# Kernel tuning notes

Measured on AMD Instinct MI355X. Metric: run time of the kernel, lower is better.

## Reference

```python
import jax, jax.numpy as jnp
import numpy as np

B, S, D = 16, 1024, 1024      # batch, seq_len (== max_ctx_k), input_dim (== embed_dim)
H = 1                          # num_heads (module's v-reshape requires 1)
E = 1024                       # embed_dim
TEMP = 1.0
EPS = 1e-12


def setup_inputs() -> dict:
    key = jax.random.key(0)
    ks = jax.random.split(key, 10)
    x = jax.random.normal(ks[0], (B, S, D), dtype=jnp.float32)
    mask = jax.random.randint(ks[1], (B, S, S), 0, 2, dtype=jnp.int32)
    # parameters (xavier-ish scales)
    Wqkv = jax.random.normal(ks[2], (2 * E, D), dtype=jnp.float32) * (1.0 / np.sqrt(D))
    bqkv = jax.random.normal(ks[3], (2 * E,), dtype=jnp.float32) * 0.02
    Wctx = jax.random.normal(ks[4], (2 * S, S), dtype=jnp.float32) * (1.0 / np.sqrt(S))
    bctx = jax.random.normal(ks[5], (2 * S,), dtype=jnp.float32) * 0.02
    Wf = jax.random.normal(ks[6], (1, 2), dtype=jnp.float32)
    bf = jax.random.normal(ks[7], (1,), dtype=jnp.float32) * 0.02
    Wo = jax.random.normal(ks[8], (D, 2 * D), dtype=jnp.float32) * (1.0 / np.sqrt(2 * D))
    bo = jax.random.normal(ks[9], (D,), dtype=jnp.float32) * 0.02
    return {"x": x, "mask": mask, "Wqkv": Wqkv, "bqkv": bqkv, "Wctx": Wctx,
            "bctx": bctx, "Wf": Wf, "bf": bf, "Wo": Wo, "bo": bo}


def reference(x, mask, Wqkv, bqkv, Wctx, bctx, Wf, bf, Wo, bo):
    head_dim = E // H
    # qkv projection -> (B, H, S, 2*head_dim)
    qkv = (jnp.einsum('bsd,ed->bse', x, Wqkv) + bqkv)
    qkv = qkv.reshape(B, S, H, 2 * head_dim).transpose(0, 2, 1, 3)
    q, k = jnp.split(qkv, 2, axis=-1)
    # v is just x per head (num_heads == 1)
    v = x.reshape(B, S, H, D).transpose(0, 2, 1, 3)          # (B, H, S, D)
    # self-attention scores (NOT scaled by sqrt(d_k), faithful to source)
    self_attn = jnp.einsum('bhqd,bhkd->bhqk', q, k)           # (B, H, S, S)
    # adjacency-derived context scores
    adj = jnp.einsum('bqd,bkd->bqk', x, x)[:, None]           # (B, 1, S, S)
    ctx_qk = jnp.einsum('bhqs,ts->bhqt', adj, Wctx) + bctx    # (B, 1, S, 2S)
    ctx_q, ctx_k = jnp.split(ctx_qk, 2, axis=-1)
    ctx_q = ctx_q / jnp.maximum(jnp.linalg.norm(ctx_q, axis=-1, keepdims=True), EPS)
    ctx_k = ctx_k / jnp.maximum(jnp.linalg.norm(ctx_k, axis=-1, keepdims=True), EPS)
    ctx_attn = jnp.einsum('bhqs,bhks->bhqk', ctx_q, ctx_k)    # (B, 1, S, S)
    # learned fuse of the two score maps: Linear(2 -> 1)
    attn = self_attn * Wf[0, 0] + ctx_attn * Wf[0, 1] + bf[0]
    attn = jax.nn.softmax(attn / TEMP, axis=-1)
    # post-softmax masking + L1 renorm
    m = (mask[:, None] != 0)                                  # (B, 1, S, S)
    attn = jnp.where(m, attn, 0.0)
    attn = attn / jnp.maximum(jnp.sum(jnp.abs(attn), axis=-1, keepdims=True), EPS)
    # value matmul and output projection
    values = jnp.einsum('bhqk,bhkd->bhqd', attn, v)           # (B, H, S, D)
    values = values.transpose(0, 2, 1, 3).reshape(B, S, D)
    o = jnp.einsum('bse,de->bsd', jnp.concatenate([x, values], axis=-1), Wo) + bo
    return o
```

## Files before the change

### kernel.cpp

```cpp
#include <hip/hip_runtime.h>
#include <hip/hip_bf16.h>

#define BB 16
#define SS 1024
#define DD 1024

typedef __hip_bfloat16 bf;
using s8v   = __attribute__((ext_vector_type(8))) short;
using f32x4 = __attribute__((ext_vector_type(4))) float;
using u16x4 = __attribute__((ext_vector_type(4))) unsigned short;

__device__ __forceinline__ void gload16(const bf* g, unsigned short* l)
{
    __builtin_amdgcn_global_load_lds(
        (const __attribute__((address_space(1))) void*)g,
        (__attribute__((address_space(3))) void*)l,
        16, 0, 0);
}

template <int EP>
__global__ __launch_bounds__(512, 2) void gemm256(
    const bf* __restrict__ A, long sA, int lda, int segA,
    const bf* __restrict__ B, long sB, int ldb, int segB,
    float* __restrict__ C, bf* __restrict__ Cb,
    bf* __restrict__ qp, bf* __restrict__ kp,
    long sC, int ldc, int K,
    const float* __restrict__ bias,
    const float* __restrict__ alpha_ptr, int alpha_idx,
    const float* __restrict__ addc_ptr,
    int accumulate)
{
    __shared__ __align__(16) unsigned short lds[65536];
    unsigned short* Asm = lds;
    unsigned short* Bsm = lds + 32768;

    const int gx = gridDim.x, gy = gridDim.y;
    const int nwg = gx * gy * (int)gridDim.z;
    int lid = blockIdx.x + gx * (blockIdx.y + gy * blockIdx.z);
    lid = (lid & 7) * (nwg >> 3) + (lid >> 3);
    const int bx = lid % gx;
    const int rem = lid / gx;
    const int by = rem % gy;
    const int bz = rem / gy;

    const int tid = threadIdx.x;
    const int w = tid >> 6, l = tid & 63;
    const int wm = w >> 2, wn = w & 3;
    const int lm = l & 15, quad = l >> 4;
    const int bh = wn >> 1;
    const int bl0 = (wn & 1) * 64;

    const int m0 = by * 256, n0 = bx * 256;
    const bf* Ab = A + (long)bz * sA;
    const bf* Bb = B + (long)bz * sB;

    const int srow = w * 16 + (l >> 3);
    const int scol = ((l & 7) ^ (l >> 3)) << 3;
    const long aoff0 = (long)srow * lda + scol;
    const long aoff1 = (long)(srow + 8) * lda + scol;
    const long boff0 = (long)srow * ldb + scol;
    const long boff1 = (long)(srow + 8) * ldb + scol;
    const int ldst = w * 1024;

    auto stageA = [&](int tt, int h) {
        const int kk = ((tt & 15) << 6) +
                       ((((unsigned)segA >> ((tt >> 4) << 3)) & 0xffu) << 10);
        const bf* g = Ab + (long)(m0 + h * 128) * lda + kk;
        unsigned short* d = Asm + (((tt & 1) << 1) + h) * 8192 + ldst;
        gload16(g + aoff0, d);
        gload16(g + aoff1, d + 512);
    };
    auto stageB = [&](int tt, int h) {
        const int kk = ((tt & 15) << 6) +
                       ((((unsigned)segB >> ((tt >> 4) << 3)) & 0xffu) << 10);
        const bf* g = Bb + (long)(n0 + h * 128) * ldb + kk;
        unsigned short* d = Bsm + (((tt & 1) << 1) + h) * 8192 + ldst;
        gload16(g + boff0, d);
        gload16(g + boff1, d + 512);
    };
    auto rdA = [&](int d, int rl, int ks) -> s8v {
        const int off = rl * 64 + (((ks << 5) + (quad << 3)) ^ ((rl & 7) << 3));
        return *(const s8v*)(Asm + ((d << 1) + wm) * 8192 + off);
    };
    auto rdB = [&](int d, int bl, int ks) -> s8v {
        const int off = bl * 64 + (((ks << 5) + (quad << 3)) ^ ((bl & 7) << 3));
        return *(const s8v*)(Bsm + ((d << 1) + bh) * 8192 + off);
    };

    f32x4 acc[8][4];
#pragma unroll
    for (int i = 0; i < 8; ++i)
#pragma unroll
        for (int j = 0; j < 4; ++j)
            acc[i][j] = (f32x4){0.f, 0.f, 0.f, 0.f};

    const int NT = K >> 6;

    stageA(0, 0); stageA(0, 1); stageB(0, 0); stageB(0, 1);
    asm volatile("s_waitcnt vmcnt(4)" ::: "memory");
    stageA(1, 0); stageA(1, 1); stageB(1, 0);
    asm volatile("s_waitcnt vmcnt(6)" ::: "memory");
    __builtin_amdgcn_s_barrier();

    s8v a[8], b[4];
    for (int t = 0; t < NT; ++t) {
        const int d = t & 1;
#pragma unroll
        for (int mf = 0; mf < 4; ++mf) {
            a[mf * 2]     = rdA(d, mf * 16 + lm, 0);
            a[mf * 2 + 1] = rdA(d, mf * 16 + lm, 1);
        }
#pragma unroll
        for (int nf = 0; nf < 2; ++nf) {
            b[nf * 2]     = rdB(d, bl0 + nf * 16 + lm, 0);
            b[nf * 2 + 1] = rdB(d, bl0 + nf * 16 + lm, 1);
        }
        if (t + 1 < NT) stageB(t + 1, 1);
        __builtin_amdgcn_s_barrier();
        __builtin_amdgcn_s_setprio(1);
#pragma unroll
        for (int mf = 0; mf < 4; ++mf)
#pragma unroll
            for (int nf = 0; nf < 2; ++nf) {
                acc[mf][nf] = __builtin_amdgcn_mfma_f32_16x16x32_bf16(a[mf*2],   b[nf*2],   acc[mf][nf], 0, 0, 0);
                acc[mf][nf] = __builtin_amdgcn_mfma_f32_16x16x32_bf16(a[mf*2+1], b[nf*2+1], acc[mf][nf], 0, 0, 0);
            }
        __builtin_amdgcn_s_setprio(0);
        __builtin_amdgcn_s_barrier();
#pragma unroll
        for (int nf = 0; nf < 2; ++nf) {
            b[nf * 2]     = rdB(d, bl0 + (nf + 2) * 16 + lm, 0);
            b[nf * 2 + 1] = rdB(d, bl0 + (nf + 2) * 16 + lm, 1);
        }
        __builtin_amdgcn_s_barrier();
        __builtin_amdgcn_s_setprio(1);
#pragma unroll
        for (int mf = 0; mf < 4; ++mf)
#pragma unroll
            for (int nf = 0; nf < 2; ++nf) {
                acc[mf][nf+2] = __builtin_amdgcn_mfma_f32_16x16x32_bf16(a[mf*2],   b[nf*2],   acc[mf][nf+2], 0, 0, 0);
                acc[mf][nf+2] = __builtin_amdgcn_mfma_f32_16x16x32_bf16(a[mf*2+1], b[nf*2+1], acc[mf][nf+2], 0, 0, 0);
            }
        __builtin_amdgcn_s_setprio(0);
        __builtin_amdgcn_s_barrier();
#pragma unroll
        for (int mf = 0; mf < 4; ++mf) {
            a[mf * 2]     = rdA(d, 64 + mf * 16 + lm, 0);
            a[mf * 2 + 1] = rdA(d, 64 + mf * 16 + lm, 1);
        }
        if (t + 2 < NT) { stageA(t + 2, 0); stageA(t + 2, 1); }
        __builtin_amdgcn_s_barrier();
        __builtin_amdgcn_s_setprio(1);
#pragma unroll
        for (int mf = 0; mf < 4; ++mf)
#pragma unroll
            for (int nf = 0; nf < 2; ++nf) {
                acc[mf+4][nf+2] = __builtin_amdgcn_mfma_f32_16x16x32_bf16(a[mf*2],   b[nf*2],   acc[mf+4][nf+2], 0, 0, 0);
                acc[mf+4][nf+2] = __builtin_amdgcn_mfma_f32_16x16x32_bf16(a[mf*2+1], b[nf*2+1], acc[mf+4][nf+2], 0, 0, 0);
            }
        __builtin_amdgcn_s_setprio(0);
        __builtin_amdgcn_s_barrier();
#pragma unroll
        for (int nf = 0; nf < 2; ++nf) {
            b[nf * 2]     = rdB(d, bl0 + nf * 16 + lm, 0);
            b[nf * 2 + 1] = rdB(d, bl0 + nf * 16 + lm, 1);
        }
        if (t + 2 < NT) {
            stageB(t + 2, 0);
            asm volatile("s_waitcnt vmcnt(6)" ::: "memory");
        } else {
            asm volatile("s_waitcnt vmcnt(0)" ::: "memory");
        }
        __builtin_amdgcn_s_barrier();
        __builtin_amdgcn_s_setprio(1);
#pragma unroll
        for (int mf = 0; mf < 4; ++mf)
#pragma unroll
            for (int nf = 0; nf < 2; ++nf) {
                acc[mf+4][nf] = __builtin_amdgcn_mfma_f32_16x16x32_bf16(a[mf*2],   b[nf*2],   acc[mf+4][nf], 0, 0, 0);
                acc[mf+4][nf] = __builtin_amdgcn_mfma_f32_16x16x32_bf16(a[mf*2+1], b[nf*2+1], acc[mf+4][nf], 0, 0, 0);
            }
        __builtin_amdgcn_s_setprio(0);
        __builtin_amdgcn_s_barrier();
    }

    const float alpha = alpha_ptr ? alpha_ptr[alpha_idx] : 1.0f;
    const float addc  = addc_ptr ? addc_ptr[0] : 0.0f;
    float* Cp = C ? C + (long)bz * sC : nullptr;
    bf* Cbp = (EP == 1) ? Cb + (long)bz * sC : nullptr;
    bf* qpz = (EP == 2 || EP == 3) ? qp + (long)bz * sC : nullptr;
    bf* kpz = (EP == 2 || EP == 3) ? kp + (long)bz * sC : nullptr;

#pragma unroll
    for (int mf = 0; mf < 8; ++mf) {
#pragma unroll
        for (int nf = 0; nf < 4; ++nf) {
            const int cidx = n0 + wn * 64 + nf * 16 + lm;
            const float bv = bias ? bias[cidx] : 0.0f;
            const long rbase = m0 + wm * 128 + mf * 16 + quad * 4;
#pragma unroll
            for (int r = 0; r < 4; ++r) {
                const long row = rbase + r;
                if (EP == 2) {
                    float v = acc[mf][nf][r] + bv;
                    if (cidx < 1024) {
                        v *= alpha;
                        bf hi = __float2bfloat16(v);
                        bf lo = __float2bfloat16(v - __bfloat162float(hi));
                        qpz[row * 3072 + cidx] = hi;
                        qpz[row * 3072 + 1024 + cidx] = lo;
                    } else {
                        const int c = cidx - 1024;
                        bf hi = __float2bfloat16(v);
                        bf lo = __float2bfloat16(v - __bfloat162float(hi));
                        kpz[row * 3072 + c] = hi;
                        kpz[row * 3072 + 1024 + c] = lo;
                    }
                } else if (EP == 3) {
                    const float v = acc[mf][nf][r] + bv;
                    const bf h = __float2bfloat16(v);
                    if (cidx < 1024) qpz[row * 3072 + 2048 + cidx] = h;
                    else             kpz[row * 3072 + 2048 + (cidx - 1024)] = h;
                } else {
                    float v = alpha * acc[mf][nf][r] + addc + bv;
                    const long off = row * (long)ldc + cidx;
                    if (EP == 1) {
                        Cbp[off] = __float2bfloat16(v);
                    } else {
                        if (accumulate) v += Cp[off];
                        Cp[off] = v;
                    }
                }
            }
        }
    }
}

__device__ inline float blockReduceSum(float v, float* red)
{
#pragma unroll
    for (int off = 32; off > 0; off >>= 1) v += __shfl_xor(v, off, 64);
    __syncthreads();
    if ((threadIdx.x & 63) == 0) red[threadIdx.x >> 6] = v;
    __syncthreads();
    return red[0] + red[1] + red[2] + red[3];
}

__device__ inline float blockReduceMax(float v, float* red)
{
#pragma unroll
    for (int off = 32; off > 0; off >>= 1) v = fmaxf(v, __shfl_xor(v, off, 64));
    __syncthreads();
    if ((threadIdx.x & 63) == 0) red[threadIdx.x >> 6] = v;
    __syncthreads();
    return fmaxf(fmaxf(red[0], red[1]), fmaxf(red[2], red[3]));
}

__device__ inline void split_bf16(float v, bf& hi, bf& lo)
{
    hi = __float2bfloat16(v);
    lo = __float2bfloat16(v - __bfloat162float(hi));
}

__global__ __launch_bounds__(256) void prep_wqkv_kernel(
    const float* __restrict__ W, bf* __restrict__ wq2)
{
    long i = (long)blockIdx.x * 256 + threadIdx.x;
    long r = i >> 10; int c = (int)(i & 1023);
    bf hi, lo; split_bf16(W[i], hi, lo);
    wq2[r * 2048 + c] = hi;
    wq2[r * 2048 + 1024 + c] = lo;
}

__global__ __launch_bounds__(256) void conv_kernel(
    const float* __restrict__ src, bf* __restrict__ dst, int cols, int src_ld, long n)
{
    long i = (long)blockIdx.x * 256 + threadIdx.x;
    if (i >= n) return;
    long r = i / cols; int c = (int)(i % cols);
    dst[i] = __float2bfloat16(src[r * src_ld + c]);
}

__global__ __launch_bounds__(256) void conv_x_kernel(
    const float* __restrict__ x, bf* __restrict__ xhl, bf* __restrict__ xT1)
{
    __shared__ float t[32][33];
    const int b = blockIdx.z;
    const int c0 = blockIdx.x * 32, r0 = blockIdx.y * 32;
    const int tx = threadIdx.x & 31, ty = threadIdx.x >> 5;
    const float* xb = x + (long)b * SS * DD;
    bf* xhlb = xhl + (long)b * SS * 2048;
#pragma unroll
    for (int p = 0; p < 4; ++p) {
        const int r = ty + 8 * p;
        const float v = xb[(long)(r0 + r) * DD + c0 + tx];
        t[r][tx] = v;
        bf hi, lo; split_bf16(v, hi, lo);
        xhlb[(long)(r0 + r) * 2048 + c0 + tx] = hi;
        xhlb[(long)(r0 + r) * 2048 + 1024 + c0 + tx] = lo;
    }
    __syncthreads();
#pragma unroll
    for (int p = 0; p < 4; ++p) {
        const int rr = ty + 8 * p;
        xT1[(long)b * DD * SS + (long)(c0 + rr) * SS + r0 + tx] =
            __float2bfloat16(t[tx][rr]);
    }
}

__global__ __launch_bounds__(256) void l2norm_fuse_kernel(
    bf* __restrict__ q3, bf* __restrict__ k3, const float* __restrict__ Wf)
{
    __shared__ float red[4];
    const long row = blockIdx.x >> 1;
    const int half = blockIdx.x & 1;
    bf* p = (half ? k3 : q3) + row * 3072 + 2048;
    const int t = threadIdx.x;

    const u16x4 u = *reinterpret_cast<const u16x4*>(p + 4 * t);
    float v[4];
    float ss = 0.0f;
#pragma unroll
    for (int i = 0; i < 4; ++i) {
        unsigned short us = u[i];
        v[i] = __bfloat162float(*reinterpret_cast<const bf*>(&us));
        ss = fmaf(v[i], v[i], ss);
    }
    ss = blockReduceSum(ss, red);
    const float inv = 1.0f / fmaxf(sqrtf(ss), 1e-12f);
    const float scale = half ? inv : inv * Wf[1];
    u16x4 o;
#pragma unroll
    for (int i = 0; i < 4; ++i) {
        bf h = __float2bfloat16(v[i] * scale);
        o[i] = *reinterpret_cast<unsigned short*>(&h);
    }
    *reinterpret_cast<u16x4*>(p + 4 * t) = o;
}

__global__ __launch_bounds__(256) void softmax_mask_kernel(
    const float* __restrict__ attn, const int* __restrict__ mask, bf* __restrict__ attn_bf)
{
    __shared__ float red[4];
    const long row = blockIdx.x;
    const float* p = attn + row * SS;
    const int* mrow = mask + row * SS;
    bf* o = attn_bf + row * SS;
    const int t = threadIdx.x;

    float v[4];
    int mv[4];
#pragma unroll
    for (int i = 0; i < 4; ++i) { v[i] = p[t + 256 * i]; mv[i] = mrow[t + 256 * i]; }
    float mx = fmaxf(fmaxf(v[0], v[1]), fmaxf(v[2], v[3]));
    mx = blockReduceMax(mx, red);

    float e[4];
    float s = 0.0f;
#pragma unroll
    for (int i = 0; i < 4; ++i) { e[i] = expf(v[i] - mx); s += e[i]; }
    s = blockReduceSum(s, red);

    float l1 = 0.0f;
#pragma unroll
    for (int i = 0; i < 4; ++i) { e[i] = mv[i] ? e[i] / s : 0.0f; l1 += e[i]; }
    l1 = blockReduceSum(l1, red);
    const float inv = 1.0f / fmaxf(l1, 1e-12f);
#pragma unroll
    for (int i = 0; i < 4; ++i) o[t + 256 * i] = __float2bfloat16(e[i] * inv);
}

extern "C" void kernel_launch(void* const* d_in, const int* in_sizes, int n_in,
                              void* d_out, int out_size, void* d_ws, size_t ws_size,
                              hipStream_t stream)
{
    const float* x    = (const float*)d_in[0];
    const int*   mask = (const int*)d_in[1];
    const float* Wqkv = (const float*)d_in[2];
    const float* bqkv = (const float*)d_in[3];
    const float* Wctx = (const float*)d_in[4];
    const float* bctx = (const float*)d_in[5];
    const float* Wf   = (const float*)d_in[6];
    const float* bfp  = (const float*)d_in[7];
    const float* Wo   = (const float*)d_in[8];
    const float* bo   = (const float*)d_in[9];
    float* out = (float*)d_out;

    const long SD = (long)SS * DD;

    auto align_up = [](size_t v) { return (v + 255) & ~(size_t)255; };

    const size_t sz_wq2  = 2048L * 2048 * 2;
    const size_t sz_wctx = 2048L * 1024 * 2;
    const size_t sz_wob  = 1024L * 2048 * 2;
    const size_t SH = align_up(sz_wq2) + align_up(sz_wctx) + align_up(sz_wob);

    const size_t szXL = 1024L * 2048 * 2;
    const size_t szXT = 1024L * 1024 * 2;
    const size_t szQ3 = 1024L * 3072 * 2;
    const size_t szY  = 2048L * 1024 * 2;
    const size_t PB = align_up(szXL) + align_up(szXT) + 2 * align_up(szQ3) +
                      align_up(szY);

    int G = 16;
    while (G > 1 && SH + (size_t)G * PB > ws_size) G >>= 1;

    char* p = (char*)d_ws;
    auto take = [&](size_t bytes) { char* r = p; p += align_up(bytes); return r; };
    bf* Wq2   = (bf*)take(sz_wq2);
    bf* Wctx1 = (bf*)take(sz_wctx);
    bf* Wob   = (bf*)take(sz_wob);
    char* RX = take((size_t)G * szXL);
    char* RT = take((size_t)G * szXT);
    char* RQ = take((size_t)G * szQ3);
    char* RK = take((size_t)G * szQ3);
    char* RY = take((size_t)G * szY);

    bf*    xhl   = (bf*)RX;
    bf*    xT1   = (bf*)RT;
    bf*    Q3    = (bf*)RQ;
    bf*    K3    = (bf*)RK;
    bf*    Y1    = (bf*)RY;
    float* attn  = (float*)RY;
    bf*    attnb = (bf*)RQ;

    const dim3 blk(256);
    const dim3 blk5(512);
    const long sXL = 1024L * 2048;
    const long sAT = 1024L * 1024;
    const long sQ3 = 1024L * 3072;
    const long sY  = 2048L * 1024;

    const int segQKV_A = 0x0100;
    const int segQKV_B = 0x010000;
    const int segATT_A = 0x02010000;
    const int segATT_B = 0x02000100;
    const int segOUT   = 0x0100;

    prep_wqkv_kernel<<<dim3((2048L * 1024) / 256), blk, 0, stream>>>(Wqkv, Wq2);
    conv_kernel<<<dim3((2048L * 1024) / 256), blk, 0, stream>>>(Wctx, Wctx1, 1024, 1024, 2048L * 1024);
    conv_kernel<<<dim3((1024L * 2048) / 256), blk, 0, stream>>>(Wo, Wob, 2048, 2048, 1024L * 2048);

    for (int bc0 = 0; bc0 < BB; bc0 += G) {
        const float* xb = x + (long)bc0 * SD;
        const int M = G * 1024;

        conv_x_kernel<<<dim3(32, 32, G), blk, 0, stream>>>(xb, xhl, xT1);

        gemm256<2><<<dim3(2048 / 256, M / 256), blk5, 0, stream>>>(
            xhl, 0, 2048, segQKV_A, Wq2, 0, 2048, segQKV_B,
            nullptr, nullptr, Q3, K3, 0, 0, 3072,
            bqkv, Wf, 0, nullptr, 0);

        gemm256<1><<<dim3(1024 / 256, 2048 / 256, G), blk5, 0, stream>>>(
            Wctx1, 0, 1024, 0, xT1, sAT, 1024, 0,
            nullptr, Y1, nullptr, nullptr, sY, 1024, 1024,
            nullptr, nullptr, 0, nullptr, 0);

        gemm256<3><<<dim3(2048 / 256, 1024 / 256, G), blk5, 0, stream>>>(
            xhl, sXL, 2048, 0, Y1, sY, 1024, 0,
            nullptr, nullptr, Q3, K3, sQ3, 0, 1024,
            bctx, nullptr, 0, nullptr, 0);

        l2norm_fuse_kernel<<<dim3(G * 1024 * 2), blk, 0, stream>>>(Q3, K3, Wf);

        gemm256<0><<<dim3(1024 / 256, 1024 / 256, G), blk5, 0, stream>>>(
            Q3, sQ3, 3072, segATT_A, K3, sQ3, 3072, segATT_B,
            attn, nullptr, nullptr, nullptr, sAT, 1024, 4096,
            nullptr, nullptr, 0, bfp, 0);

        softmax_mask_kernel<<<dim3(G * 1024), blk, 0, stream>>>(
            attn, mask + (long)bc0 * SS * SS, attnb);

        gemm256<1><<<dim3(1024 / 256, 1024 / 256, G), blk5, 0, stream>>>(
            attnb, sAT, 1024, 0, xT1, sAT, 1024, 0,
            nullptr, xhl + 1024, nullptr, nullptr, sXL, 2048, 1024,
            nullptr, nullptr, 0, nullptr, 0);

        gemm256<0><<<dim3(1024 / 256, M / 256), blk5, 0, stream>>>(
            xhl, 0, 2048, segOUT, Wob, 0, 2048, segOUT,
            out + (long)bc0 * SD, nullptr, nullptr, nullptr, 0, 1024, 2048,
            bo, nullptr, 0, nullptr, 0);
    }
}
```

Measured before the change: 1.013 ms.

## Reassociate context GEMM chain and vectorize conversion and softmax kernels

The context path used to compute Y = Wctx·xᵀ (2048x1024 per batch) and then x·Y. It now computes adj = x·xᵀ (1024x1024, bf16 hi part only) and then adj·Wctxᵀ, which reorders the matrix products and halves the intermediate size and the FLOPs of the first GEMM. Separately, the weight conversion, x split/transpose, and softmax kernels now use 4- or 8-wide vector loads and stores with larger tiles. The reassociation rounds adj to bf16 before the second GEMM, which can change numerical accuracy of the context scores.

Result: no change. 1.004 ms (-0.9%).

```diff
diff --git a/kernel.cpp b/kernel.cpp
--- a/kernel.cpp
+++ b/kernel.cpp
@@ -9,6 +9,8 @@
 using s8v   = __attribute__((ext_vector_type(8))) short;
 using f32x4 = __attribute__((ext_vector_type(4))) float;
 using u16x4 = __attribute__((ext_vector_type(4))) unsigned short;
+using u16x8 = __attribute__((ext_vector_type(8))) unsigned short;
+using i32x4 = __attribute__((ext_vector_type(4))) int;
 
 __device__ __forceinline__ void gload16(const bf* g, unsigned short* l)
 {
@@ -262,49 +264,80 @@
     lo = __float2bfloat16(v - __bfloat162float(hi));
 }
 
+__device__ __forceinline__ unsigned short bf_bits(float v)
+{
+    bf h = __float2bfloat16(v);
+    return *reinterpret_cast<unsigned short*>(&h);
+}
+
 __global__ __launch_bounds__(256) void prep_wqkv_kernel(
     const float* __restrict__ W, bf* __restrict__ wq2)
 {
-    long i = (long)blockIdx.x * 256 + threadIdx.x;
-    long r = i >> 10; int c = (int)(i & 1023);
-    bf hi, lo; split_bf16(W[i], hi, lo);
-    wq2[r * 2048 + c] = hi;
-    wq2[r * 2048 + 1024 + c] = lo;
+    const long i4 = ((long)blockIdx.x * 256 + threadIdx.x) * 4;
+    const long r = i4 >> 10; const int c = (int)(i4 & 1023);
+    const f32x4 s = *(const f32x4*)&W[i4];
+    u16x4 h4, l4;
+#pragma unroll
+    for (int j = 0; j < 4; ++j) {
+        bf hi, lo; split_bf16(s[j], hi, lo);
+        h4[j] = *reinterpret_cast<unsigned short*>(&hi);
+        l4[j] = *reinterpret_cast<unsigned short*>(&lo);
+    }
+    *(u16x4*)&wq2[r * 2048 + c] = h4;
+    *(u16x4*)&wq2[r * 2048 + 1024 + c] = l4;
 }
 
 __global__ __launch_bounds__(256) void conv_kernel(
     const float* __restrict__ src, bf* __restrict__ dst, int cols, int src_ld, long n)
 {
-    long i = (long)blockIdx.x * 256 + threadIdx.x;
-    if (i >= n) return;
-    long r = i / cols; int c = (int)(i % cols);
-    dst[i] = __float2bfloat16(src[r * src_ld + c]);
+    const long i4 = ((long)blockIdx.x * 256 + threadIdx.x) * 4;
+    if (i4 >= n) return;
+    const long r = i4 / cols; const int c = (int)(i4 % cols);
+    const f32x4 s = *(const f32x4*)&src[r * src_ld + c];
+    u16x4 d4;
+#pragma unroll
+    for (int j = 0; j < 4; ++j) d4[j] = bf_bits(s[j]);
+    *(u16x4*)&dst[i4] = d4;
 }
 
 __global__ __launch_bounds__(256) void conv_x_kernel(
     const float* __restrict__ x, bf* __restrict__ xhl, bf* __restrict__ xT1)
 {
-    __shared__ float t[32][33];
+    __shared__ float t[64][65];
     const int b = blockIdx.z;
-    const int c0 = blockIdx.x * 32, r0 = blockIdx.y * 32;
-    const int tx = threadIdx.x & 31, ty = threadIdx.x >> 5;
+    const int c0 = blockIdx.x * 64, r0 = blockIdx.y * 64;
+    const int tx = threadIdx.x & 7, ty = threadIdx.x >> 3;
     const float* xb = x + (long)b * SS * DD;
     bf* xhlb = xhl + (long)b * SS * 2048;
 #pragma unroll
-    for (int p = 0; p < 4; ++p) {
-        const int r = ty + 8 * p;
-        const float v = xb[(long)(r0 + r) * DD + c0 + tx];
-        t[r][tx] = v;
-        bf hi, lo; split_bf16(v, hi, lo);
-        xhlb[(long)(r0 + r) * 2048 + c0 + tx] = hi;
-        xhlb[(long)(r0 + r) * 2048 + 1024 + c0 + tx] = lo;
+    for (int p = 0; p < 2; ++p) {
+        const int r = ty + 32 * p;
+        const f32x4 v0 = *(const f32x4*)&xb[(long)(r0 + r) * DD + c0 + tx * 8];
+        const f32x4 v1 = *(const f32x4*)&xb[(long)(r0 + r) * DD + c0 + tx * 8 + 4];
+        u16x8 hv, lv;
+#pragma unroll
+        for (int j = 0; j < 4; ++j) {
+            bf hi, lo;
+            split_bf16(v0[j], hi, lo);
+            hv[j] = *reinterpret_cast<unsigned short*>(&hi);
+            lv[j] = *reinterpret_cast<unsigned short*>(&lo);
+            t[r][tx * 8 + j] = v0[j];
+            split_bf16(v1[j], hi, lo);
+            hv[j + 4] = *reinterpret_cast<unsigned short*>(&hi);
+            lv[j + 4] = *reinterpret_cast<unsigned short*>(&lo);
+            t[r][tx * 8 + 4 + j] = v1[j];
+        }
+        *(u16x8*)&xhlb[(long)(r0 + r) * 2048 + c0 + tx * 8] = hv;
+        *(u16x8*)&xhlb[(long)(r0 + r) * 2048 + 1024 + c0 + tx * 8] = lv;
     }
     __syncthreads();
 #pragma unroll
-    for (int p = 0; p < 4; ++p) {
-        const int rr = ty + 8 * p;
-        xT1[(long)b * DD * SS + (long)(c0 + rr) * SS + r0 + tx] =
-            __float2bfloat16(t[tx][rr]);
+    for (int p = 0; p < 2; ++p) {
+        const int dd = ty + 32 * p;
+        u16x8 o;
+#pragma unroll
+        for (int j = 0; j < 8; ++j) o[j] = bf_bits(t[tx * 8 + j][dd]);
+        *(u16x8*)&xT1[(long)b * DD * SS + (long)(c0 + dd) * SS + r0 + tx * 8] = o;
     }
 }
 
@@ -331,10 +364,7 @@
     const float scale = half ? inv : inv * Wf[1];
     u16x4 o;
 #pragma unroll
-    for (int i = 0; i < 4; ++i) {
-        bf h = __float2bfloat16(v[i] * scale);
-        o[i] = *reinterpret_cast<unsigned short*>(&h);
-    }
+    for (int i = 0; i < 4; ++i) o[i] = bf_bits(v[i] * scale);
     *reinterpret_cast<u16x4*>(p + 4 * t) = o;
 }
 
@@ -343,15 +373,11 @@
 {
     __shared__ float red[4];
     const long row = blockIdx.x;
-    const float* p = attn + row * SS;
-    const int* mrow = mask + row * SS;
+    const int t4 = threadIdx.x * 4;
+    const f32x4 v = *(const f32x4*)(attn + row * SS + t4);
+    const i32x4 mv = *(const i32x4*)(mask + row * SS + t4);
     bf* o = attn_bf + row * SS;
-    const int t = threadIdx.x;
-
-    float v[4];
-    int mv[4];
-#pragma unroll
-    for (int i = 0; i < 4; ++i) { v[i] = p[t + 256 * i]; mv[i] = mrow[t + 256 * i]; }
+
     float mx = fmaxf(fmaxf(v[0], v[1]), fmaxf(v[2], v[3]));
     mx = blockReduceMax(mx, red);
 
@@ -366,8 +392,10 @@
     for (int i = 0; i < 4; ++i) { e[i] = mv[i] ? e[i] / s : 0.0f; l1 += e[i]; }
     l1 = blockReduceSum(l1, red);
     const float inv = 1.0f / fmaxf(l1, 1e-12f);
-#pragma unroll
-    for (int i = 0; i < 4; ++i) o[t + 256 * i] = __float2bfloat16(e[i] * inv);
+    u16x4 ov;
+#pragma unroll
+    for (int i = 0; i < 4; ++i) ov[i] = bf_bits(e[i] * inv);
+    *(u16x4*)(o + t4) = ov;
 }
 
 extern "C" void kernel_launch(void* const* d_in, const int* in_sizes, int n_in,
@@ -398,7 +426,7 @@
     const size_t szXL = 1024L * 2048 * 2;
     const size_t szXT = 1024L * 1024 * 2;
     const size_t szQ3 = 1024L * 3072 * 2;
-    const size_t szY  = 2048L * 1024 * 2;
+    const size_t szY  = 1024L * 1024 * 4;
     const size_t PB = align_up(szXL) + align_up(szXT) + 2 * align_up(szQ3) +
                       align_up(szY);
 
@@ -420,7 +448,7 @@
     bf*    xT1   = (bf*)RT;
     bf*    Q3    = (bf*)RQ;
     bf*    K3    = (bf*)RK;
-    bf*    Y1    = (bf*)RY;
+    bf*    adjb  = (bf*)RY;
     float* attn  = (float*)RY;
     bf*    attnb = (bf*)RQ;
 
@@ -429,7 +457,6 @@
     const long sXL = 1024L * 2048;
     const long sAT = 1024L * 1024;
     const long sQ3 = 1024L * 3072;
-    const long sY  = 2048L * 1024;
 
     const int segQKV_A = 0x0100;
     const int segQKV_B = 0x010000;
@@ -437,28 +464,28 @@
     const int segATT_B = 0x02000100;
     const int segOUT   = 0x0100;
 
-    prep_wqkv_kernel<<<dim3((2048L * 1024) / 256), blk, 0, stream>>>(Wqkv, Wq2);
-    conv_kernel<<<dim3((2048L * 1024) / 256), blk, 0, stream>>>(Wctx, Wctx1, 1024, 1024, 2048L * 1024);
-    conv_kernel<<<dim3((1024L * 2048) / 256), blk, 0, stream>>>(Wo, Wob, 2048, 2048, 1024L * 2048);
+    prep_wqkv_kernel<<<dim3((2048L * 1024) / 1024), blk, 0, stream>>>(Wqkv, Wq2);
+    conv_kernel<<<dim3((2048L * 1024) / 1024), blk, 0, stream>>>(Wctx, Wctx1, 1024, 1024, 2048L * 1024);
+    conv_kernel<<<dim3((1024L * 2048) / 1024), blk, 0, stream>>>(Wo, Wob, 2048, 2048, 1024L * 2048);
 
     for (int bc0 = 0; bc0 < BB; bc0 += G) {
         const float* xb = x + (long)bc0 * SD;
         const int M = G * 1024;
 
-        conv_x_kernel<<<dim3(32, 32, G), blk, 0, stream>>>(xb, xhl, xT1);
+        conv_x_kernel<<<dim3(16, 16, G), blk, 0, stream>>>(xb, xhl, xT1);
 
         gemm256<2><<<dim3(2048 / 256, M / 256), blk5, 0, stream>>>(
             xhl, 0, 2048, segQKV_A, Wq2, 0, 2048, segQKV_B,
             nullptr, nullptr, Q3, K3, 0, 0, 3072,
             bqkv, Wf, 0, nullptr, 0);
 
-        gemm256<1><<<dim3(1024 / 256, 2048 / 256, G), blk5, 0, stream>>>(
-            Wctx1, 0, 1024, 0, xT1, sAT, 1024, 0,
-            nullptr, Y1, nullptr, nullptr, sY, 1024, 1024,
+        gemm256<1><<<dim3(1024 / 256, 1024 / 256, G), blk5, 0, stream>>>(
+            xhl, sXL, 2048, 0, xhl, sXL, 2048, 0,
+            nullptr, adjb, nullptr, nullptr, sAT, 1024, 1024,
             nullptr, nullptr, 0, nullptr, 0);
 
         gemm256<3><<<dim3(2048 / 256, 1024 / 256, G), blk5, 0, stream>>>(
-            xhl, sXL, 2048, 0, Y1, sY, 1024, 0,
+            adjb, sAT, 1024, 0, Wctx1, 0, 1024, 0,
             nullptr, nullptr, Q3, K3, sQ3, 0, 1024,
             bctx, nullptr, 0, nullptr, 0);
 
```
